# Optimization experiments

Measured on AMD Instinct MI355X. Metric: run time of the kernel, lower is better.

Reference implementation:

```python
import jax, jax.numpy as jnp
import numpy as np

N, E, L, HID, HEADS, G = 50000, 800000, 2, 128, 8, 256
DK = HID // HEADS

def _ln(x, g, b, eps=1e-5):
    m = jnp.mean(x, axis=-1, keepdims=True)
    v = jnp.mean((x - m) ** 2, axis=-1, keepdims=True)
    return (x - m) * jax.lax.rsqrt(v + eps) * g + b

def setup_inputs() -> dict:
    key = jax.random.key(0)
    ks = jax.random.split(key, 24)
    rn = lambda i, s: (0.05 * jax.random.normal(ks[i], s)).astype(jnp.float32)
    return {
        'node_attr': jax.random.randint(ks[0], (N, 4), 0, 64, dtype=jnp.int32),
        'batch_idx': jnp.sort(jax.random.randint(ks[1], (N,), 0, G, dtype=jnp.int32)),
        'edge_index': jax.random.randint(ks[2], (2, E), 0, N, dtype=jnp.int32),
        'strat_dist': jax.random.randint(ks[3], (E,), 0, 32, dtype=jnp.int32),
        'strat_path': jax.random.randint(ks[4], (E,), 0, 16, dtype=jnp.int32),
        'atom_emb': rn(5, (4, 64, HID)),
        'dist_emb': rn(6, (L, 32, HID)),
        'path_emb': rn(7, (L, 16, HID)),
        'Wq': rn(8, (L, HID, HID)), 'bq': rn(9, (L, HID)),
        'Wk': rn(10, (L, HID, HID)), 'bk': rn(11, (L, HID)),
        'Wv': rn(12, (L, HID, HID)), 'bv': rn(13, (L, HID)),
        'Wa': rn(14, (L, HID, HID)), 'ba': rn(15, (L, HID)),
        'ln1_g': jnp.ones((L, HID), jnp.float32), 'ln1_b': jnp.zeros((L, HID), jnp.float32),
        'Wmid': rn(16, (L, HID, 2 * HID)), 'bmid': rn(17, (L, 2 * HID)),
        'Wo': rn(18, (L, 2 * HID, HID)), 'bo': rn(19, (L, HID)),
        'ln2_g': jnp.ones((L, HID), jnp.float32), 'ln2_b': jnp.zeros((L, HID), jnp.float32),
        'W_out': rn(20, (HID, 1)), 'b_out': jnp.zeros((1,), jnp.float32),
    }

def reference(node_attr, batch_idx, edge_index, strat_dist, strat_path,
              atom_emb, dist_emb, path_emb, Wq, bq, Wk, bk, Wv, bv, Wa, ba,
              ln1_g, ln1_b, Wmid, bmid, Wo, bo, ln2_g, ln2_b, W_out, b_out):
    # node encoder: sum of per-feature embeddings (AtomEncoder style)
    x = sum(atom_emb[f][node_attr[:, f]] for f in range(node_attr.shape[1]))  # [N, HID]
    src, tgt = edge_index[0], edge_index[1]  # j (source), i (target)
    inv_sqrt_dk = np.float32(1.0 / np.sqrt(DK))
    for l in range(L):
        # per-edge gather + relational encodings added to the source vector
        s = x[src] + dist_emb[l][strat_dist] + path_emb[l][strat_path]  # [E, HID]
        t = x[tgt]                                                      # [E, HID]
        q = (t @ Wq[l] + bq[l]).reshape(E, HEADS, DK)
        k = (s @ Wk[l] + bk[l]).reshape(E, HEADS, DK)
        v = (s @ Wv[l] + bv[l]).reshape(E, HEADS, DK)
        scores = jnp.sum(q * k, axis=-1) * inv_sqrt_dk  # [E, HEADS]
        # segment softmax keyed on target node id
        smax = jax.ops.segment_max(scores, tgt, num_segments=N)
        ex = jnp.exp(scores - smax[tgt])
        den = jax.ops.segment_sum(ex, tgt, num_segments=N)
        att = ex / (den[tgt] + 1e-16)                   # [E, HEADS]
        msg = (v * att[:, :, None]).reshape(E, HID)
        aggr = jax.ops.segment_sum(msg, tgt, num_segments=N)  # scatter-add
        # update: attn FFN + residual + LayerNorms (dropout is identity in eval)
        h = _ln(jax.nn.gelu(aggr, approximate=False) @ Wa[l] + ba[l] + x, ln1_g[l], ln1_b[l])
        h2 = jax.nn.gelu(h @ Wmid[l] + bmid[l], approximate=False) @ Wo[l] + bo[l]
        x = _ln(h2 + h, ln2_g[l], ln2_b[l])
    # global mean pool per graph, then readout
    cnt = jax.ops.segment_sum(jnp.ones((N,), x.dtype), batch_idx, num_segments=G)
    pooled = jax.ops.segment_sum(x, batch_idx, num_segments=G) / jnp.maximum(cnt, 1.0)[:, None]
    return pooled @ W_out + b_out
```

## Files before the change

kernel.cpp:

```cpp
#include <hip/hip_runtime.h>
#include <hip/hip_bf16.h>
#include <math.h>
#include <stdint.h>

#define N_NODES 50000
#define N_EDGES 800000
#define HID 128
#define NGRAPH 256
#define NLAYER 2
#define CAP 64

#define SCATH 782
#define EHALF 400000

typedef __bf16 bf16x8 __attribute__((ext_vector_type(8)));
typedef __bf16 bf16x2 __attribute__((ext_vector_type(2)));
typedef float f32x4 __attribute__((ext_vector_type(4)));
typedef float f32x2 __attribute__((ext_vector_type(2)));

__device__ __forceinline__ float gelu_f(float v) {
    return 0.5f * v * (1.0f + erff(v * 0.70710678118654752f));
}

__device__ __forceinline__ void cvt4_fp8(uint32_t w, float* o) {
    f32x2 lo = __builtin_amdgcn_cvt_pk_f32_fp8(w, false);
    f32x2 hi = __builtin_amdgcn_cvt_pk_f32_fp8(w, true);
    o[0] = lo[0]; o[1] = lo[1]; o[2] = hi[0]; o[3] = hi[1];
}
__device__ __forceinline__ uint32_t pk4_fp8(float a, float b, float c, float d) {
    int w = __builtin_amdgcn_cvt_pk_fp8_f32(a, b, 0, false);
    w = __builtin_amdgcn_cvt_pk_fp8_f32(c, d, w, true);
    return (uint32_t)w;
}

__device__ __forceinline__ void scatter_block(
    int blk, int ebase, int elim,
    const int* __restrict__ tgt, const int* __restrict__ src,
    const int* __restrict__ sd, const int* __restrict__ sp,
    int* __restrict__ cnt, uint32_t* __restrict__ ei) {
    int tid = threadIdx.x;
    int e0 = ebase + blk * 512 + tid;
    int e1 = e0 + 256;
    bool v0 = e0 < elim;
    bool v1 = e1 < elim;
    int t0 = 0, t1 = 0;
    uint32_t p0 = 0, p1 = 0;
    if (v0) {
        t0 = tgt[e0];
        p0 = (uint32_t)src[e0] | ((uint32_t)((sd[e0] << 4) | sp[e0]) << 16);
    }
    if (v1) {
        t1 = tgt[e1];
        p1 = (uint32_t)src[e1] | ((uint32_t)((sd[e1] << 4) | sp[e1]) << 16);
    }
    int r0 = CAP, r1 = CAP;
    if (v0) r0 = atomicAdd(&cnt[t0], 1);
    if (v1) r1 = atomicAdd(&cnt[t1], 1);
    if (v0 && r0 < CAP) ei[(t0 << 6) + r0] = p0;
    if (v1 && r1 < CAP) ei[(t1 << 6) + r1] = p1;
}

__global__ __launch_bounds__(256) void prep_kernel(
    const int* __restrict__ attr, const float* __restrict__ aemb,
    __bf16* __restrict__ xb,
    const float* __restrict__ de, const float* __restrict__ pe,
    const float* __restrict__ Wk, const float* __restrict__ Wv,
    __bf16* __restrict__ tkv,
    const float* __restrict__ Wq, const float* __restrict__ Wa,
    const float* __restrict__ Wmid, const float* __restrict__ Wo,
    __bf16* __restrict__ wqkvf, __bf16* __restrict__ waf,
    __bf16* __restrict__ wmidf, __bf16* __restrict__ wof,
    const int* __restrict__ batch, const float* __restrict__ bout,
    const float* __restrict__ bq, const float* __restrict__ bk,
    const float* __restrict__ bv,
    float* __restrict__ invc, float* __restrict__ outp, float* __restrict__ bqkv,
    const int* __restrict__ tgt, const int* __restrict__ src,
    const int* __restrict__ sd, const int* __restrict__ sp,
    int* __restrict__ cnt, uint32_t* __restrict__ ei) {
    __shared__ float sde[128];
    int b = blockIdx.x;
    int tid = threadIdx.x;
    if (b < SCATH) {
        scatter_block(b, 0, EHALF, tgt, src, sd, sp, cnt, ei);
        return;
    }
    b -= SCATH;
    if (b < 25000) {
        int idx = b * 256 + tid;
        int n = idx >> 7, c = idx & 127;
        const int4 a = *(const int4*)(attr + n * 4);
        float s = aemb[(0 * 64 + a.x) * 128 + c] + aemb[(1 * 64 + a.y) * 128 + c] +
                  aemb[(2 * 64 + a.z) * 128 + c] + aemb[(3 * 64 + a.w) * 128 + c];
        xb[idx] = (__bf16)s;
    } else if (b < 26024) {
        int bb = b - 25000;
        int l = bb >> 9;
        int md = bb & 511;
        int dd = md >> 4, pp = md & 15;
        int c = tid;
        if (c < 128) sde[c] = de[l * 4096 + dd * 128 + c] + pe[l * 2048 + pp * 128 + c];
        __syncthreads();
        const float* W = (c < 128) ? (Wk + l * 16384) : (Wv + l * 16384);
        int cc = c & 127;
        float acc = 0.f;
#pragma unroll 4
        for (int k = 0; k < 128; k++) acc = fmaf(sde[k], W[k * 128 + cc], acc);
        tkv[(size_t)bb * 256 + c] = (__bf16)acc;
    } else if (b < 26152) {
        int u = (b - 26024) * 256 + tid;
        int l = u >> 14, r = u & 16383;
        const float* srcp;
        __bf16* dstp;
        int kg, scol, srcCO;
        if (r < 6144) {
            kg = r / 384;
            int uu = r % 384;
            int sec = uu >> 7, cc = uu & 127;
            scol = ((cc & 15) << 3) | (cc >> 4);
            const float* Ws = (sec == 0) ? Wq : (sec == 1) ? Wk : Wv;
            srcp = Ws + l * 16384;
            srcCO = 128;
            dstp = wqkvf + (size_t)l * 49152 + (size_t)r * 8;
        } else if (r < 8192) {
            int rr = r - 6144;
            kg = rr >> 7;
            int cc = rr & 127;
            scol = ((cc & 15) << 3) | (cc >> 4);
            srcp = Wa + l * 16384;
            srcCO = 128;
            dstp = waf + (size_t)l * 16384 + (size_t)rr * 8;
        } else if (r < 12288) {
            int rr = r - 8192;
            kg = rr >> 8;
            int uu = rr & 255;
            int blk = uu >> 7, cc = uu & 127;
            scol = blk * 128 + (((cc & 15) << 3) | (cc >> 4));
            srcp = Wmid + l * 32768;
            srcCO = 256;
            dstp = wmidf + (size_t)l * 32768 + (size_t)rr * 8;
        } else {
            int rr = r - 12288;
            kg = rr >> 7;
            int cc = rr & 127;
            scol = ((cc & 15) << 3) | (cc >> 4);
            srcp = Wo + l * 32768;
            srcCO = 128;
            dstp = wof + (size_t)l * 32768 + (size_t)rr * 8;
        }
        bf16x8 o;
#pragma unroll
        for (int j = 0; j < 8; j++) o[j] = (__bf16)srcp[(kg * 8 + j) * srcCO + scol];
        *(bf16x8*)dstp = o;
    } else {
        int sb = b - 26152;
        if (sb == 0) {
            int g = tid;
            int lo = 0, hi = N_NODES;
            while (lo < hi) { int mid = (lo + hi) >> 1; if (batch[mid] < g) lo = mid + 1; else hi = mid; }
            int start = lo;
            lo = start; hi = N_NODES;
            while (lo < hi) { int mid = (lo + hi) >> 1; if (batch[mid] < g + 1) lo = mid + 1; else hi = mid; }
            int c2 = lo - start;
            invc[g] = 1.0f / fmaxf((float)c2, 1.0f);
            outp[g] = bout[0];
        } else {
            int r = (sb - 1) * 256 + tid;
            int l = r / 384, c = r % 384;
            float v = (c < 128) ? bq[l * 128 + c]
                    : (c < 256) ? bk[l * 128 + c - 128]
                                : bv[l * 128 + c - 256];
            bqkv[r] = v;
        }
    }
}

__global__ __launch_bounds__(256) void qkv_gemm(
    const __bf16* __restrict__ A, const __bf16* __restrict__ Wf,
    const float* __restrict__ bias, __bf16* __restrict__ Qb,
    uint8_t* __restrict__ kv8, int M, int scatN,
    const int* __restrict__ tgt, const int* __restrict__ src,
    const int* __restrict__ sd, const int* __restrict__ sp,
    int* __restrict__ cnt, uint32_t* __restrict__ ei) {
    int tid = threadIdx.x;
    if (blockIdx.x < (unsigned)scatN) {
        scatter_block(blockIdx.x, EHALF, N_EDGES, tgt, src, sd, sp, cnt, ei);
        return;
    }
    int bq = blockIdx.x - scatN;
    int sec = bq % 3;
    int rowblk = bq / 3;
    int lane = tid & 63;
    int wv = tid >> 6;
    int row0 = rowblk * 64 + wv * 16;
    int col0 = sec * 128;
    if (row0 >= M) return;
    int quad = lane >> 4, tq = lane & 15;
    f32x4 acc[8] = {};
#pragma unroll
    for (int k0 = 0; k0 < 128; k0 += 32) {
        int rr = row0 + tq;
        if (rr >= M) rr = M - 1;
        bf16x8 af = *(const bf16x8*)(A + (size_t)rr * 128 + k0 + quad * 8);
#pragma unroll
        for (int nt = 0; nt < 8; nt++) {
            bf16x8 bfr = *(const bf16x8*)(Wf + ((size_t)((k0 >> 3) + quad) * 384 + col0 + nt * 16 + tq) * 8);
            acc[nt] = __builtin_amdgcn_mfma_f32_16x16x32_bf16(af, bfr, acc[nt], 0, 0, 0);
        }
    }
    int cb = tq * 8;
    float bia[8];
#pragma unroll
    for (int t = 0; t < 8; t++) bia[t] = bias[col0 + cb + t];
#pragma unroll
    for (int v = 0; v < 4; v++) {
        int rr = row0 + quad * 4 + v;
        if (rr >= M) continue;
        float val[8];
#pragma unroll
        for (int t = 0; t < 8; t++) val[t] = acc[t][v] + bia[t];
        if (sec == 0) {
            bf16x8 ov;
#pragma unroll
            for (int t = 0; t < 8; t++) ov[t] = (__bf16)val[t];
            *(bf16x8*)(Qb + (size_t)rr * 128 + cb) = ov;
        } else {
            uint2 st;
            st.x = pk4_fp8(val[0], val[1], val[2], val[3]);
            st.y = pk4_fp8(val[4], val[5], val[6], val[7]);
            *(uint2*)(kv8 + (size_t)rr * 256 + (sec - 1) * 128 + cb) = st;
        }
    }
}

template <int CI, bool GOUT, bool LN, bool POOL>
__global__ __launch_bounds__(256) void mfma_gemm(
    const __bf16* __restrict__ A, const __bf16* __restrict__ Wf,
    const float* __restrict__ bias, const __bf16* __restrict__ res,
    const float* __restrict__ lng, const float* __restrict__ lnb,
    __bf16* outb,
    const int* __restrict__ batch, const float* __restrict__ invc,
    const float* __restrict__ WoutV, float* __restrict__ outp,
    int M, int CO) {
    __shared__ float ps[POOL ? NGRAPH : 1];
    int lane = threadIdx.x & 63;
    int wv = threadIdx.x >> 6;
    int row0 = blockIdx.y * 64 + wv * 16;
    int col0 = blockIdx.x * 128;
    bool active = row0 < M;
    if (POOL) {
        ps[threadIdx.x] = 0.f;
        __syncthreads();
    } else if (!active) {
        return;
    }
    int quad = lane >> 4, tq = lane & 15;
    if (active) {
        f32x4 acc[8] = {};
#pragma unroll
        for (int k0 = 0; k0 < CI; k0 += 32) {
            int rr = row0 + tq;
            if (rr >= M) rr = M - 1;
            bf16x8 af = *(const bf16x8*)(A + (size_t)rr * CI + k0 + quad * 8);
#pragma unroll
            for (int nt = 0; nt < 8; nt++) {
                bf16x8 bfr = *(const bf16x8*)(Wf + ((size_t)((k0 >> 3) + quad) * CO + col0 + nt * 16 + tq) * 8);
                acc[nt] = __builtin_amdgcn_mfma_f32_16x16x32_bf16(af, bfr, acc[nt], 0, 0, 0);
            }
        }
        int cb = col0 + tq * 8;
        float bia[8] = {};
        if (bias) {
#pragma unroll
            for (int t = 0; t < 8; t++) bia[t] = bias[cb + t];
        }
        float gv[8], bv2[8];
        if (LN) {
#pragma unroll
            for (int t = 0; t < 8; t++) { gv[t] = lng[cb + t]; bv2[t] = lnb[cb + t]; }
        }
        float wo8[8];
        if (POOL) {
#pragma unroll
            for (int t = 0; t < 8; t++) wo8[t] = WoutV[cb + t];
        }
#pragma unroll
        for (int v = 0; v < 4; v++) {
            int rr = row0 + quad * 4 + v;
            if (rr >= M) continue;
            float val[8];
#pragma unroll
            for (int nt = 0; nt < 8; nt++) val[nt] = acc[nt][v] + bia[nt];
            if (res) {
                bf16x8 rv = *(const bf16x8*)(res + (size_t)rr * 128 + tq * 8);
#pragma unroll
                for (int t = 0; t < 8; t++) val[t] += (float)rv[t];
            }
            if (GOUT) {
#pragma unroll
                for (int t = 0; t < 8; t++) val[t] = gelu_f(val[t]);
            }
            if (LN) {
                float s = 0.f, s2 = 0.f;
#pragma unroll
                for (int t = 0; t < 8; t++) { s += val[t]; s2 = fmaf(val[t], val[t], s2); }
#pragma unroll
                for (int o = 1; o < 16; o <<= 1) {
                    s += __shfl_xor(s, o);
                    s2 += __shfl_xor(s2, o);
                }
                float m = s * (1.0f / 128.0f);
                float var = s2 * (1.0f / 128.0f) - m * m;
                float rs = rsqrtf(var + 1e-5f);
#pragma unroll
                for (int t = 0; t < 8; t++) val[t] = (val[t] - m) * rs * gv[t] + bv2[t];
            }
            if (outb) {
                bf16x8 ov;
#pragma unroll
                for (int t = 0; t < 8; t++) ov[t] = (__bf16)val[t];
                *(bf16x8*)(outb + (size_t)rr * CO + cb) = ov;
            }
            if (POOL) {
                float dot = 0.f;
#pragma unroll
                for (int t = 0; t < 8; t++) dot = fmaf(val[t], wo8[t], dot);
#pragma unroll
                for (int o = 1; o < 16; o <<= 1) dot += __shfl_xor(dot, o);
                if (tq == 0) {
                    int g = batch[rr];
                    atomicAdd(&ps[g], dot * invc[g]);
                }
            }
        }
    }
    if (POOL) {
        __syncthreads();
        float pv = ps[threadIdx.x];
        if (pv != 0.f) atomicAdd(&outp[threadIdx.x], pv);
    }
}

__global__ __launch_bounds__(256) void attn_kernel(
    const __bf16* __restrict__ Qb, const uint8_t* __restrict__ kv8,
    const __bf16* __restrict__ tkv,
    const int* __restrict__ cnt, const uint32_t* __restrict__ ei,
    __bf16* __restrict__ outb) {
    __shared__ float red[4][1376];
    int wv = threadIdx.x >> 6;
    int i = blockIdx.x * 4 + wv;
    int lane = threadIdx.x & 63;
    int slot = lane >> 3, h = lane & 7;
    int ch0 = h * 16;
    const __bf16* qp = Qb + (size_t)i * 128 + ch0;
    bf16x8 q0 = *(const bf16x8*)qp;
    bf16x8 q1 = *(const bf16x8*)(qp + 8);
    float qf[16];
#pragma unroll
    for (int t = 0; t < 8; t++) { qf[t] = (float)q0[t]; qf[8 + t] = (float)q1[t]; }
    int deg = cnt[i];
    if (deg > CAP) deg = CAP;
    int p0 = i << 6;
    int p1 = p0 + deg;
    float l = 0.f;
    float a[16] = {};
    int p = p0 + slot;
    uint32_t w1 = 0, w2 = 0;
    if (p < p1) w1 = ei[p];
    if (p + 8 < p1) w2 = ei[p + 8];
    uint4 kw, vw;
    bf16x8 t0, t1, u0, u1;
    {
        int j = w1 & 0xffff, md = w1 >> 16;
        const uint8_t* kr = kv8 + (size_t)j * 256 + ch0;
        kw = *(const uint4*)kr;
        vw = *(const uint4*)(kr + 128);
        const __bf16* tr = tkv + md * 256 + ch0;
        t0 = *(const bf16x8*)tr;
        t1 = *(const bf16x8*)(tr + 8);
        u0 = *(const bf16x8*)(tr + 128);
        u1 = *(const bf16x8*)(tr + 136);
    }
    while (p < p1) {
        uint4 kwn, vwn;
        bf16x8 t0n, t1n, u0n, u1n;
        {
            int j = w2 & 0xffff, md = w2 >> 16;
            const uint8_t* kr = kv8 + (size_t)j * 256 + ch0;
            kwn = *(const uint4*)kr;
            vwn = *(const uint4*)(kr + 128);
            const __bf16* tr = tkv + md * 256 + ch0;
            t0n = *(const bf16x8*)tr;
            t1n = *(const bf16x8*)(tr + 8);
            u0n = *(const bf16x8*)(tr + 128);
            u1n = *(const bf16x8*)(tr + 136);
        }
        uint32_t w3 = w2;
        if (p + 16 < p1) w3 = ei[p + 16];
        float kf[16], vf[16];
        cvt4_fp8(kw.x, kf + 0); cvt4_fp8(kw.y, kf + 4);
        cvt4_fp8(kw.z, kf + 8); cvt4_fp8(kw.w, kf + 12);
        cvt4_fp8(vw.x, vf + 0); cvt4_fp8(vw.y, vf + 4);
        cvt4_fp8(vw.z, vf + 8); cvt4_fp8(vw.w, vf + 12);
        float s = 0.f;
#pragma unroll
        for (int t = 0; t < 8; t++) {
            s = fmaf(qf[t], kf[t] + (float)t0[t], s);
            s = fmaf(qf[8 + t], kf[8 + t] + (float)t1[t], s);
        }
        float pe = __expf(s * 0.25f);
        l += pe;
#pragma unroll
        for (int t = 0; t < 8; t++) {
            a[t] = fmaf(pe, vf[t] + (float)u0[t], a[t]);
            a[8 + t] = fmaf(pe, vf[8 + t] + (float)u1[t], a[8 + t]);
        }
        kw = kwn; vw = vwn; t0 = t0n; t1 = t1n; u0 = u0n; u1 = u1n;
        w2 = w3;
        p += 8;
    }
    float* rw = red[wv] + slot * 172 + 20 * h;
    *(float4*)(rw + 0) = make_float4(a[0], a[1], a[2], a[3]);
    *(float4*)(rw + 4) = make_float4(a[4], a[5], a[6], a[7]);
    *(float4*)(rw + 8) = make_float4(a[8], a[9], a[10], a[11]);
    *(float4*)(rw + 12) = make_float4(a[12], a[13], a[14], a[15]);
    red[wv][slot * 172 + 156 + h] = l;
    asm volatile("" ::: "memory");
    int pc = 2 * lane + 4 * (lane >> 3);
    int hh = lane >> 3;
    float s0 = 0.f, s1 = 0.f, ls = 0.f;
#pragma unroll
    for (int s = 0; s < 8; s++) {
        float2 v = *(const float2*)(red[wv] + s * 172 + pc);
        s0 += v.x;
        s1 += v.y;
        ls += red[wv][s * 172 + 156 + hh];
    }
    float inv = 1.0f / (ls + 1e-16f);
    bf16x2 o2;
    o2[0] = (__bf16)gelu_f(s0 * inv);
    o2[1] = (__bf16)gelu_f(s1 * inv);
    *(bf16x2*)(outb + (size_t)i * 128 + 2 * lane) = o2;
}

extern "C" void kernel_launch(void* const* d_in, const int* in_sizes, int n_in,
                              void* d_out, int out_size, void* d_ws, size_t ws_size,
                              hipStream_t stream) {
    const int N = N_NODES, E = N_EDGES;
    const int* node_attr = (const int*)d_in[0];
    const int* batch_idx = (const int*)d_in[1];
    const int* edge_index = (const int*)d_in[2];
    const int* strat_dist = (const int*)d_in[3];
    const int* strat_path = (const int*)d_in[4];
    const float* atom_emb = (const float*)d_in[5];
    const float* dist_emb = (const float*)d_in[6];
    const float* path_emb = (const float*)d_in[7];
    const float* Wq = (const float*)d_in[8];
    const float* bq = (const float*)d_in[9];
    const float* Wk = (const float*)d_in[10];
    const float* bk = (const float*)d_in[11];
    const float* Wv = (const float*)d_in[12];
    const float* bv = (const float*)d_in[13];
    const float* Wa = (const float*)d_in[14];
    const float* ba = (const float*)d_in[15];
    const float* ln1g = (const float*)d_in[16];
    const float* ln1b = (const float*)d_in[17];
    const float* Wmid = (const float*)d_in[18];
    const float* bmid = (const float*)d_in[19];
    const float* Wo = (const float*)d_in[20];
    const float* bo = (const float*)d_in[21];
    const float* ln2g = (const float*)d_in[22];
    const float* ln2b = (const float*)d_in[23];
    const float* Wout = (const float*)d_in[24];
    const float* bout = (const float*)d_in[25];
    float* out = (float*)d_out;

    const int* src = edge_index;
    const int* tgt = edge_index + E;

    size_t NF = (size_t)N * HID;
    float* invc = (float*)d_ws;
    float* bqkv = invc + 256;
    __bf16* xb = (__bf16*)(bqkv + 768);
    __bf16* Qb = xb + NF;
    __bf16* ab = Qb + NF;
    __bf16* midb = ab + NF;
    __bf16* tkv = midb + 2 * NF;
    __bf16* wqkvf = tkv + 262144;
    __bf16* waf = wqkvf + 98304;
    __bf16* wmidf = waf + 32768;
    __bf16* wof = wmidf + 65536;
    uint8_t* kv8 = (uint8_t*)(wof + 65536);
    uint32_t* ei = (uint32_t*)(kv8 + (size_t)N * 256);
    int* cnt = (int*)(ei + (size_t)N * CAP);

    hipMemsetAsync(cnt, 0, N * sizeof(int), stream);
    prep_kernel<<<SCATH + 26156, 256, 0, stream>>>(
        node_attr, atom_emb, xb,
        dist_emb, path_emb, Wk, Wv, tkv,
        Wq, Wa, Wmid, Wo, wqkvf, waf, wmidf, wof,
        batch_idx, bout, bq, bk, bv, invc, out, bqkv,
        tgt, src, strat_dist, strat_path, cnt, ei);

    const int GB = (N + 63) / 64;
    const int AB = (N + 3) / 4;

    for (int l = 0; l < NLAYER; ++l) {
        int scatN = (l == 0) ? SCATH : 0;
        qkv_gemm<<<scatN + 3 * GB, 256, 0, stream>>>(
            xb, wqkvf + l * 49152, bqkv + l * 384, Qb, kv8, N, scatN,
            tgt, src, strat_dist, strat_path, cnt, ei);

        attn_kernel<<<AB, 256, 0, stream>>>(Qb, kv8, tkv + l * 131072, cnt, ei, ab);

        mfma_gemm<128, false, true, false><<<dim3(1, GB), 256, 0, stream>>>(
            ab, waf + l * 16384, ba + l * 128, xb, ln1g + l * 128, ln1b + l * 128,
            ab, nullptr, nullptr, nullptr, nullptr, N, 128);
        mfma_gemm<128, true, false, false><<<dim3(2, GB), 256, 0, stream>>>(
            ab, wmidf + l * 32768, bmid + l * 256, nullptr, nullptr, nullptr,
            midb, nullptr, nullptr, nullptr, nullptr, N, 256);
        if (l < NLAYER - 1) {
            mfma_gemm<256, false, true, false><<<dim3(1, GB), 256, 0, stream>>>(
                midb, wof + l * 32768, bo + l * 128, ab, ln2g + l * 128, ln2b + l * 128,
                xb, nullptr, nullptr, nullptr, nullptr, N, 128);
        } else {
            mfma_gemm<256, false, true, true><<<dim3(1, GB), 256, 0, stream>>>(
                midb, wof + l * 32768, bo + l * 128, ab, ln2g + l * 128, ln2b + l * 128,
                nullptr, batch_idx, invc, Wout, out, N, 128);
        }
    }
}
```

Baseline: 431.8 us.

## Pad edge counters, vectorize node encoder, store relational tables in fp32

Spaces each per-node edge counter 32 ints (128 bytes) apart so concurrent atomics land on separate cache lines. This raises the memset to 6.4 MB. The node encoder now has each thread produce 8 channels with vector loads, so it needs 8x fewer blocks. The dist/path K/V table is kept in fp32 instead of bf16, which removes the conversions in the attention inner loop but doubles the gathered bytes per edge for that table.

```diff
diff --git a/kernel.cpp b/kernel.cpp
--- a/kernel.cpp
+++ b/kernel.cpp
@@ -12,6 +12,13 @@
 
 #define SCATH 782
 #define EHALF 400000
+
+#define CPAD 5
+
+#define ENC_B 3125
+#define TKV_B (ENC_B + 1024)
+#define RPK_B (TKV_B + 128)
+#define PREP_B (RPK_B + 4)
 
 typedef __bf16 bf16x8 __attribute__((ext_vector_type(8)));
 typedef __bf16 bf16x2 __attribute__((ext_vector_type(2)));
@@ -54,8 +61,8 @@
         p1 = (uint32_t)src[e1] | ((uint32_t)((sd[e1] << 4) | sp[e1]) << 16);
     }
     int r0 = CAP, r1 = CAP;
-    if (v0) r0 = atomicAdd(&cnt[t0], 1);
-    if (v1) r1 = atomicAdd(&cnt[t1], 1);
+    if (v0) r0 = atomicAdd(&cnt[t0 << CPAD], 1);
+    if (v1) r1 = atomicAdd(&cnt[t1 << CPAD], 1);
     if (v0 && r0 < CAP) ei[(t0 << 6) + r0] = p0;
     if (v1 && r1 < CAP) ei[(t1 << 6) + r1] = p1;
 }
@@ -65,7 +72,7 @@
     __bf16* __restrict__ xb,
     const float* __restrict__ de, const float* __restrict__ pe,
     const float* __restrict__ Wk, const float* __restrict__ Wv,
-    __bf16* __restrict__ tkv,
+    float* __restrict__ tkv,
     const float* __restrict__ Wq, const float* __restrict__ Wa,
     const float* __restrict__ Wmid, const float* __restrict__ Wo,
     __bf16* __restrict__ wqkvf, __bf16* __restrict__ waf,
@@ -85,15 +92,28 @@
         return;
     }
     b -= SCATH;
-    if (b < 25000) {
-        int idx = b * 256 + tid;
-        int n = idx >> 7, c = idx & 127;
+    if (b < ENC_B) {
+        int gid = b * 256 + tid;
+        int n = gid >> 4;
+        int c8 = (gid & 15) << 3;
         const int4 a = *(const int4*)(attr + n * 4);
-        float s = aemb[(0 * 64 + a.x) * 128 + c] + aemb[(1 * 64 + a.y) * 128 + c] +
-                  aemb[(2 * 64 + a.z) * 128 + c] + aemb[(3 * 64 + a.w) * 128 + c];
-        xb[idx] = (__bf16)s;
-    } else if (b < 26024) {
-        int bb = b - 25000;
+        const float* r0 = aemb + (size_t)(0 * 64 + a.x) * 128 + c8;
+        const float* r1 = aemb + (size_t)(1 * 64 + a.y) * 128 + c8;
+        const float* r2 = aemb + (size_t)(2 * 64 + a.z) * 128 + c8;
+        const float* r3 = aemb + (size_t)(3 * 64 + a.w) * 128 + c8;
+        f32x4 v0a = *(const f32x4*)r0, v0b = *(const f32x4*)(r0 + 4);
+        f32x4 v1a = *(const f32x4*)r1, v1b = *(const f32x4*)(r1 + 4);
+        f32x4 v2a = *(const f32x4*)r2, v2b = *(const f32x4*)(r2 + 4);
+        f32x4 v3a = *(const f32x4*)r3, v3b = *(const f32x4*)(r3 + 4);
+        bf16x8 o;
+#pragma unroll
+        for (int j = 0; j < 4; j++) {
+            o[j] = (__bf16)(v0a[j] + v1a[j] + v2a[j] + v3a[j]);
+            o[4 + j] = (__bf16)(v0b[j] + v1b[j] + v2b[j] + v3b[j]);
+        }
+        *(bf16x8*)(xb + (size_t)n * 128 + c8) = o;
+    } else if (b < TKV_B) {
+        int bb = b - ENC_B;
         int l = bb >> 9;
         int md = bb & 511;
         int dd = md >> 4, pp = md & 15;
@@ -105,9 +125,9 @@
         float acc = 0.f;
 #pragma unroll 4
         for (int k = 0; k < 128; k++) acc = fmaf(sde[k], W[k * 128 + cc], acc);
-        tkv[(size_t)bb * 256 + c] = (__bf16)acc;
-    } else if (b < 26152) {
-        int u = (b - 26024) * 256 + tid;
+        tkv[(size_t)bb * 256 + c] = acc;
+    } else if (b < RPK_B) {
+        int u = (b - TKV_B) * 256 + tid;
         int l = u >> 14, r = u & 16383;
         const float* srcp;
         __bf16* dstp;
@@ -152,7 +172,7 @@
         for (int j = 0; j < 8; j++) o[j] = (__bf16)srcp[(kg * 8 + j) * srcCO + scol];
         *(bf16x8*)dstp = o;
     } else {
-        int sb = b - 26152;
+        int sb = b - RPK_B;
         if (sb == 0) {
             int g = tid;
             int lo = 0, hi = N_NODES;
@@ -342,7 +362,7 @@
 
 __global__ __launch_bounds__(256) void attn_kernel(
     const __bf16* __restrict__ Qb, const uint8_t* __restrict__ kv8,
-    const __bf16* __restrict__ tkv,
+    const float* __restrict__ tkv,
     const int* __restrict__ cnt, const uint32_t* __restrict__ ei,
     __bf16* __restrict__ outb) {
     __shared__ float red[4][1376];
@@ -357,7 +377,7 @@
     float qf[16];
 #pragma unroll
     for (int t = 0; t < 8; t++) { qf[t] = (float)q0[t]; qf[8 + t] = (float)q1[t]; }
-    int deg = cnt[i];
+    int deg = cnt[i << CPAD];
     if (deg > CAP) deg = CAP;
     int p0 = i << 6;
     int p1 = p0 + deg;
@@ -368,31 +388,33 @@
     if (p < p1) w1 = ei[p];
     if (p + 8 < p1) w2 = ei[p + 8];
     uint4 kw, vw;
-    bf16x8 t0, t1, u0, u1;
+    f32x4 tt[4], uu[4];
     {
         int j = w1 & 0xffff, md = w1 >> 16;
         const uint8_t* kr = kv8 + (size_t)j * 256 + ch0;
         kw = *(const uint4*)kr;
         vw = *(const uint4*)(kr + 128);
-        const __bf16* tr = tkv + md * 256 + ch0;
-        t0 = *(const bf16x8*)tr;
-        t1 = *(const bf16x8*)(tr + 8);
-        u0 = *(const bf16x8*)(tr + 128);
-        u1 = *(const bf16x8*)(tr + 136);
+        const float* tr = tkv + md * 256 + ch0;
+#pragma unroll
+        for (int t = 0; t < 4; t++) {
+            tt[t] = *(const f32x4*)(tr + 4 * t);
+            uu[t] = *(const f32x4*)(tr + 128 + 4 * t);
+        }
     }
     while (p < p1) {
         uint4 kwn, vwn;
-        bf16x8 t0n, t1n, u0n, u1n;
+        f32x4 ttn[4], uun[4];
         {
             int j = w2 & 0xffff, md = w2 >> 16;
             const uint8_t* kr = kv8 + (size_t)j * 256 + ch0;
             kwn = *(const uint4*)kr;
             vwn = *(const uint4*)(kr + 128);
-            const __bf16* tr = tkv + md * 256 + ch0;
-            t0n = *(const bf16x8*)tr;
-            t1n = *(const bf16x8*)(tr + 8);
-            u0n = *(const bf16x8*)(tr + 128);
-            u1n = *(const bf16x8*)(tr + 136);
+            const float* tr = tkv + md * 256 + ch0;
+#pragma unroll
+            for (int t = 0; t < 4; t++) {
+                ttn[t] = *(const f32x4*)(tr + 4 * t);
+                uun[t] = *(const f32x4*)(tr + 128 + 4 * t);
+            }
         }
         uint32_t w3 = w2;
         if (p + 16 < p1) w3 = ei[p + 16];
@@ -403,18 +425,14 @@
         cvt4_fp8(vw.z, vf + 8); cvt4_fp8(vw.w, vf + 12);
         float s = 0.f;
 #pragma unroll
-        for (int t = 0; t < 8; t++) {
-            s = fmaf(qf[t], kf[t] + (float)t0[t], s);
-            s = fmaf(qf[8 + t], kf[8 + t] + (float)t1[t], s);
-        }
+        for (int t = 0; t < 16; t++) s = fmaf(qf[t], kf[t] + tt[t >> 2][t & 3], s);
         float pe = __expf(s * 0.25f);
         l += pe;
 #pragma unroll
-        for (int t = 0; t < 8; t++) {
-            a[t] = fmaf(pe, vf[t] + (float)u0[t], a[t]);
-            a[8 + t] = fmaf(pe, vf[8 + t] + (float)u1[t], a[8 + t]);
-        }
-        kw = kwn; vw = vwn; t0 = t0n; t1 = t1n; u0 = u0n; u1 = u1n;
+        for (int t = 0; t < 16; t++) a[t] = fmaf(pe, vf[t] + uu[t >> 2][t & 3], a[t]);
+        kw = kwn; vw = vwn;
+#pragma unroll
+        for (int t = 0; t < 4; t++) { tt[t] = ttn[t]; uu[t] = uun[t]; }
         w2 = w3;
         p += 8;
     }
@@ -480,12 +498,12 @@
     size_t NF = (size_t)N * HID;
     float* invc = (float*)d_ws;
     float* bqkv = invc + 256;
-    __bf16* xb = (__bf16*)(bqkv + 768);
+    float* tkvf = bqkv + 768;
+    __bf16* xb = (__bf16*)(tkvf + 262144);
     __bf16* Qb = xb + NF;
     __bf16* ab = Qb + NF;
     __bf16* midb = ab + NF;
-    __bf16* tkv = midb + 2 * NF;
-    __bf16* wqkvf = tkv + 262144;
+    __bf16* wqkvf = midb + 2 * NF;
     __bf16* waf = wqkvf + 98304;
     __bf16* wmidf = waf + 32768;
     __bf16* wof = wmidf + 65536;
@@ -493,10 +511,10 @@
     uint32_t* ei = (uint32_t*)(kv8 + (size_t)N * 256);
     int* cnt = (int*)(ei + (size_t)N * CAP);
 
-    hipMemsetAsync(cnt, 0, N * sizeof(int), stream);
-    prep_kernel<<<SCATH + 26156, 256, 0, stream>>>(
+    hipMemsetAsync(cnt, 0, (size_t)N * 32 * sizeof(int), stream);
+    prep_kernel<<<SCATH + PREP_B, 256, 0, stream>>>(
         node_attr, atom_emb, xb,
-        dist_emb, path_emb, Wk, Wv, tkv,
+        dist_emb, path_emb, Wk, Wv, tkvf,
         Wq, Wa, Wmid, Wo, wqkvf, waf, wmidf, wof,
         batch_idx, bout, bq, bk, bv, invc, out, bqkv,
         tgt, src, strat_dist, strat_path, cnt, ei);
@@ -510,7 +528,7 @@
             xb, wqkvf + l * 49152, bqkv + l * 384, Qb, kv8, N, scatN,
             tgt, src, strat_dist, strat_path, cnt, ei);
 
-        attn_kernel<<<AB, 256, 0, stream>>>(Qb, kv8, tkv + l * 131072, cnt, ei, ab);
+        attn_kernel<<<AB, 256, 0, stream>>>(Qb, kv8, tkvf + l * 131072, cnt, ei, ab);
 
         mfma_gemm<128, false, true, false><<<dim3(1, GB), 256, 0, stream>>>(
             ab, waf + l * 16384, ba + l * 128, xb, ln1g + l * 128, ln1b + l * 128,
```

Result: slower. 504.4 us (+16.8%).
